# Performance work log

Hardware: AMD Instinct MI355X
Metric: run time of the kernel (lower is better)

Reference implementation:

```python
import jax, jax.numpy as jnp
import numpy as np

ALPHA = 0.7
NUM_HEADS = 12
NUM_KV_HEADS = 6
HEAD_DIM = 64
ROPE_BASE = 10000.0


def ternary_quantize(w):
    thr = ALPHA * jnp.mean(jnp.abs(w))
    return jnp.sign(w) * (jnp.abs(w) >= thr).astype(w.dtype)


def bitlinear(x, w):
    # forward: F.linear(x, ternary(w)) * mean(|w|)
    scale = jnp.mean(jnp.abs(w))
    qw = ternary_quantize(w)
    return (x @ qw.T) * scale


def rope_tables(seq_len, dim, dtype):
    inv_freq = 1.0 / (ROPE_BASE ** (jnp.arange(0, dim, 2, dtype=jnp.float32) / dim))
    t = jnp.arange(seq_len, dtype=jnp.float32)
    freqs = jnp.outer(t, inv_freq)            # [S, dim/2]
    emb = jnp.concatenate([freqs, freqs], -1)  # [S, dim]
    return jnp.cos(emb).astype(dtype), jnp.sin(emb).astype(dtype)


def rotate_half(x):
    x1, x2 = jnp.split(x, 2, axis=-1)
    return jnp.concatenate([-x2, x1], axis=-1)


def setup_inputs() -> dict:
    key = jax.random.key(0)
    ks = jax.random.split(key, 5)
    B, S, H = 2, 2048, 768
    return {
        "hidden_states": jax.random.normal(ks[0], (B, S, H), jnp.float32),
        "Wq": jax.random.normal(ks[1], (768, 768), jnp.float32) * 0.02,
        "Wk": jax.random.normal(ks[2], (384, 768), jnp.float32) * 0.02,
        "Wv": jax.random.normal(ks[3], (384, 768), jnp.float32) * 0.02,
        "Wo": jax.random.normal(ks[4], (768, 768), jnp.float32) * 0.02,
    }


def reference(hidden_states, Wq, Wk, Wv, Wo):
    B, S, H = hidden_states.shape
    nh, nkv, hd = NUM_HEADS, NUM_KV_HEADS, HEAD_DIM
    groups = nh // nkv

    q = bitlinear(hidden_states, Wq).reshape(B, S, nh, hd).transpose(0, 2, 1, 3)
    k = bitlinear(hidden_states, Wk).reshape(B, S, nkv, hd).transpose(0, 2, 1, 3)
    v = bitlinear(hidden_states, Wv).reshape(B, S, nkv, hd).transpose(0, 2, 1, 3)

    cos, sin = rope_tables(S, hd, hidden_states.dtype)  # [S, hd]
    cos = cos[None, None]  # [1,1,S,hd]
    sin = sin[None, None]
    q = q * cos + rotate_half(q) * sin
    k = k * cos + rotate_half(k) * sin

    # GQA: expand kv heads to full head count
    k = jnp.repeat(k, groups, axis=1)  # [B, nh, S, hd]
    v = jnp.repeat(v, groups, axis=1)

    scale = 1.0 / jnp.sqrt(jnp.asarray(hd, hidden_states.dtype))
    scores = jnp.einsum("bhsd,bhtd->bhst", q, k) * scale
    attn = jax.nn.softmax(scores, axis=-1)
    out = jnp.einsum("bhst,bhtd->bhsd", attn, v)
    out = out.transpose(0, 2, 1, 3).reshape(B, S, H)
    return bitlinear(out, Wo)
```

## Files before the change

### kernel.cpp

```cpp
#include <hip/hip_runtime.h>
#include <cmath>

typedef unsigned short u16;
typedef unsigned int u32;
typedef __bf16 bf16x2 __attribute__((ext_vector_type(2)));
typedef __bf16 bf16x8 __attribute__((ext_vector_type(8)));
typedef float f32x16 __attribute__((ext_vector_type(16)));

#define NQ (768*768)
#define NK (384*768)

__device__ __forceinline__ u16 f2bf(float f) {
  u32 u = __float_as_uint(f);
  u32 r = (u + 0x7FFFu + ((u >> 16) & 1u)) >> 16;
  return (u16)r;
}
__device__ __forceinline__ u32 packbf(float a, float b) {
#if __has_builtin(__builtin_amdgcn_cvt_pk_bf16_f32)
  bf16x2 v = __builtin_amdgcn_cvt_pk_bf16_f32(a, b);
  u32 r; __builtin_memcpy(&r, &v, 4); return r;
#else
  return (u32)f2bf(a) | ((u32)f2bf(b) << 16);
#endif
}
__device__ __forceinline__ float fexp2(float x) {
#if __has_builtin(__builtin_amdgcn_exp2f)
  return __builtin_amdgcn_exp2f(x);
#else
  return exp2f(x);
#endif
}
__device__ __forceinline__ bf16x8 ldfrag(const u16* p) { bf16x8 v; __builtin_memcpy(&v, p, 16); return v; }
__device__ __forceinline__ f32x16 mfma32_(bf16x8 a, bf16x8 b, f32x16 c) {
  return __builtin_amdgcn_mfma_f32_32x32x16_bf16(a, b, c, 0, 0, 0);
}

__device__ __forceinline__ int fidx(int r, int k) {
  return (r >> 5) * 24576 + (k >> 4) * 512 + ((r & 31) + 32 * ((k >> 3) & 1)) * 8 + (k & 7);
}
__device__ __forceinline__ int kidx(int b6kvh, int s, int d) {
  return b6kvh * 131072 + (s >> 5) * 2048 + (d >> 4) * 512 +
         ((s & 31) + 32 * ((d >> 3) & 1)) * 8 + (d & 7);
}
__device__ __forceinline__ int qidx(int b, int s, int h, int d) {
  return ((b * 64 + (s >> 5)) * 12 + h) * 2048 + (d >> 4) * 512 +
         ((s & 31) + 32 * ((d >> 3) & 1)) * 8 + (d & 7);
}
__device__ __forceinline__ int vidx(int b6kvh, int d, int p) {
  return b6kvh * 131072 + (p >> 6) * 4096 + (d >> 5) * 2048 + ((p >> 4) & 3) * 512 +
         ((d & 31) + 32 * ((p >> 3) & 1)) * 8 + (p & 7);
}

__global__ __launch_bounds__(256) void abssum_kernel(const float* __restrict__ wq, const float* __restrict__ wk,
                                                     const float* __restrict__ wv, const float* __restrict__ wo,
                                                     float* __restrict__ sums) {
  int which = blockIdx.y;
  const float* w = (which == 0) ? wq : (which == 1) ? wk : (which == 2) ? wv : wo;
  int n4 = ((which == 0 || which == 3) ? NQ : NK) >> 2;
  const float4* w4 = (const float4*)w;
  float s = 0.f;
  for (int i = blockIdx.x * blockDim.x + threadIdx.x; i < n4; i += gridDim.x * blockDim.x) {
    float4 v = w4[i];
    s += fabsf(v.x) + fabsf(v.y) + fabsf(v.z) + fabsf(v.w);
  }
  for (int off = 32; off; off >>= 1) s += __shfl_down(s, off);
  __shared__ float ls[4];
  if ((threadIdx.x & 63) == 0) ls[threadIdx.x >> 6] = s;
  __syncthreads();
  if (threadIdx.x == 0) atomicAdd(&sums[which], ls[0] + ls[1] + ls[2] + ls[3]);
}

__global__ __launch_bounds__(256) void prep_kernel(const float* __restrict__ wq, const float* __restrict__ wk,
                                                   const float* __restrict__ wv, const float* __restrict__ wo,
                                                   const float* __restrict__ sums, const float* __restrict__ x,
                                                   u16* __restrict__ qw, u16* __restrict__ woq,
                                                   u16* __restrict__ xb, float2* __restrict__ rt) {
  int i = blockIdx.x * blockDim.x + threadIdx.x;
  if (i < 221184) {
    int n = i / 96, k8 = i - n * 96;
    const float* src; float th; u16* dst; int nd;
    if (n < 768)       { src = wq + n * 768;          th = 0.7f * sums[0] * (1.f / NQ); dst = qw;  nd = n; }
    else if (n < 1152) { src = wk + (n - 768) * 768;  th = 0.7f * sums[1] * (1.f / NK); dst = qw;  nd = n; }
    else if (n < 1536) { src = wv + (n - 1152) * 768; th = 0.7f * sums[2] * (1.f / NK); dst = qw;  nd = n; }
    else               { src = wo + (n - 1536) * 768; th = 0.7f * sums[3] * (1.f / NQ); dst = woq; nd = n - 1536; }
    const float4* sp = (const float4*)(src + k8 * 8);
    float4 v0 = sp[0], v1 = sp[1];
    float e[8] = {v0.x, v0.y, v0.z, v0.w, v1.x, v1.y, v1.z, v1.w};
    u16 o[8];
#pragma unroll
    for (int j = 0; j < 8; j++)
      o[j] = f2bf((fabsf(e[j]) >= th) ? ((e[j] > 0.f) ? 1.f : -1.f) : 0.f);
    __builtin_memcpy(dst + fidx(nd, k8 * 8), o, 16);
  } else if (i < 614400) {
    int j = i - 221184;
    int m = j / 96, k8 = j - m * 96;
    const float4* xp = (const float4*)(x + m * 768 + k8 * 8);
    float4 v0 = xp[0], v1 = xp[1];
    u16 o[8] = { f2bf(v0.x), f2bf(v0.y), f2bf(v0.z), f2bf(v0.w),
                 f2bf(v1.x), f2bf(v1.y), f2bf(v1.z), f2bf(v1.w) };
    __builtin_memcpy(xb + fidx(m, k8 * 8), o, 16);
  } else {
    int j = i - 614400;
    int s = j >> 5, c = j & 31;
    float f = exp2f((float)c * -0.41524101186092029f);
    float sn, cs; sincosf((float)s * f, &sn, &cs);
    rt[j] = make_float2(cs, sn);
  }
}

__global__ __launch_bounds__(256, 3) void gemm_qkv_kernel(const u16* __restrict__ xb, const u16* __restrict__ qw,
                                                          const float* __restrict__ sums,
                                                          const float2* __restrict__ rt,
                                                          u16* __restrict__ qb, u16* __restrict__ kb,
                                                          u16* __restrict__ vT) {
  int tn = blockIdx.x, tm = blockIdx.y;
  int t = threadIdx.x, lane = t & 63, w = t >> 6, c = lane & 31, g2 = lane >> 5;
  int wm = w & 1, wn = w >> 1;
  const u16* abase = xb + (tm * 2 + wm) * 24576 + lane * 8;
  const u16* bbase0 = qw + (tn * 4 + wn * 2) * 24576 + lane * 8;
  const u16* bbase1 = bbase0 + 24576;
  f32x16 acc[2]; acc[0] = (f32x16)0.f; acc[1] = (f32x16)0.f;
  bf16x8 aA[4], c0A[4], c1A[4], aB[4], c0B[4], c1B[4];
#pragma unroll
  for (int ks = 0; ks < 4; ks++) {
    aA[ks]  = ldfrag(abase + ks * 512);
    c0A[ks] = ldfrag(bbase0 + ks * 512);
    c1A[ks] = ldfrag(bbase1 + ks * 512);
  }
#pragma unroll
  for (int kk = 0; kk < 48; kk += 8) {
#pragma unroll
    for (int ks = 0; ks < 4; ks++) {
      aB[ks]  = ldfrag(abase + (kk + 4 + ks) * 512);
      c0B[ks] = ldfrag(bbase0 + (kk + 4 + ks) * 512);
      c1B[ks] = ldfrag(bbase1 + (kk + 4 + ks) * 512);
    }
#pragma unroll
    for (int ks = 0; ks < 4; ks++) {
      acc[0] = mfma32_(aA[ks], c0A[ks], acc[0]);
      acc[1] = mfma32_(aA[ks], c1A[ks], acc[1]);
    }
    if (kk + 8 < 48) {
#pragma unroll
      for (int ks = 0; ks < 4; ks++) {
        aA[ks]  = ldfrag(abase + (kk + 8 + ks) * 512);
        c0A[ks] = ldfrag(bbase0 + (kk + 8 + ks) * 512);
        c1A[ks] = ldfrag(bbase1 + (kk + 8 + ks) * 512);
      }
    }
#pragma unroll
    for (int ks = 0; ks < 4; ks++) {
      acc[0] = mfma32_(aB[ks], c0B[ks], acc[0]);
      acc[1] = mfma32_(aB[ks], c1B[ks], acc[1]);
    }
  }
  float sq = sums[0] * (1.f / NQ) * 0.180336880111120f;
  float sk = sums[1] * (1.f / NK);
  float sv = sums[2] * (1.f / NK);
  int mb = tm * 64 + wm * 32 + 4 * g2;
  if (tn < 9) {
    float sc = (tn < 6) ? sq : sk;
    int head = (tn < 6) ? (tn * 2 + wn) : ((tn - 6) * 2 + wn);
    const float2* rp = rt + c;
#pragma unroll
    for (int r = 0; r < 16; r++) {
      int m = mb + (r & 3) + 8 * (r >> 2);
      int bb = m >> 11, s = m & 2047;
      float2 cs2 = rp[s << 5];
      float x1 = acc[0][r] * sc, x2 = acc[1][r] * sc;
      u16 y1 = f2bf(x1 * cs2.x - x2 * cs2.y);
      u16 y2 = f2bf(x2 * cs2.x + x1 * cs2.y);
      if (tn < 6) {
        qb[qidx(bb, s, head, c)]      = y1;
        qb[qidx(bb, s, head, c + 32)] = y2;
      } else {
        kb[kidx(bb * 6 + head, s, c)]      = y1;
        kb[kidx(bb * 6 + head, s, c + 32)] = y2;
      }
    }
  } else {
    int kvh = (tn - 9) * 2 + wn;
#pragma unroll
    for (int nb = 0; nb < 2; nb++)
#pragma unroll
      for (int r = 0; r < 16; r++) {
        int m = mb + (r & 3) + 8 * (r >> 2);
        int bb = m >> 11, s = m & 2047;
        int sp = (s & ~12) | ((s & 4) << 1) | ((s & 8) >> 1);
        vT[vidx(bb * 6 + kvh, nb * 32 + c, sp)] = f2bf(acc[nb][r] * sv);
      }
  }
}

__device__ __forceinline__ void attn_step(const bf16x8 (&kf)[4], const bf16x8 (&vf)[2][2],
                                          const bf16x8 (&qf)[4], f32x16 (&O)[2], float& lsum) {
  f32x16 S = (f32x16)0.f;
#pragma unroll
  for (int ks = 0; ks < 4; ks++) S = mfma32_(kf[ks], qf[ks], S);
#pragma unroll
  for (int r = 0; r < 16; r++) S[r] = fexp2(S[r]);
  lsum += (((S[0] + S[1]) + (S[2] + S[3])) + ((S[4] + S[5]) + (S[6] + S[7])))
        + (((S[8] + S[9]) + (S[10] + S[11])) + ((S[12] + S[13]) + (S[14] + S[15])));
  u32 P[8];
#pragma unroll
  for (int j = 0; j < 8; j++) P[j] = packbf(S[2 * j], S[2 * j + 1]);
  bf16x8 PA0, PA1;
  __builtin_memcpy(&PA0, &P[0], 16);
  __builtin_memcpy(&PA1, &P[4], 16);
  O[0] = mfma32_(PA0, vf[0][0], O[0]);
  O[1] = mfma32_(PA0, vf[1][0], O[1]);
  O[0] = mfma32_(PA1, vf[0][1], O[0]);
  O[1] = mfma32_(PA1, vf[1][1], O[1]);
}

__global__ __launch_bounds__(256, 3) void attn_kernel(const u16* __restrict__ qb, const u16* __restrict__ kb,
                                                      const u16* __restrict__ vT, u16* __restrict__ ab) {
  __shared__ float Obuf[4][32][66];
  __shared__ float Lbuf[4][32];
  int bk = blockIdx.x;
  int b = bk / 6, kvh = bk % 6;
  int qp = blockIdx.y & 31, h2 = blockIdx.y >> 5;
  int h = kvh * 2 + h2;
  int t = threadIdx.x, lane = t & 63, w = t >> 6, c = lane & 31, g2 = lane >> 5;

  const u16* q0 = qb + ((b * 64 + qp * 2) * 12 + h) * 2048 + lane * 8;
  const u16* q1 = q0 + 12 * 2048;
  bf16x8 qf0[4], qf1[4];
#pragma unroll
  for (int ks = 0; ks < 4; ks++) { qf0[ks] = ldfrag(q0 + ks * 512); qf1[ks] = ldfrag(q1 + ks * 512); }

  f32x16 fz = (f32x16)0.f;
  f32x16 O0[2] = {fz, fz}, O1[2] = {fz, fz};
  float lsum0 = 0.f, lsum1 = 0.f;

  const u16* Kb = kb + bk * 131072;
  const u16* Vb = vT + bk * 131072;

  for (int it = 0; it < 16; ++it) {
    int g = w * 16 + it;
    const u16* kt = Kb + g * 2048 + lane * 8;
    const u16* vt = Vb + (g >> 1) * 4096 + (g & 1) * 1024 + lane * 8;
    bf16x8 kf[4], vf[2][2];
#pragma unroll
    for (int ks = 0; ks < 4; ks++) kf[ks] = ldfrag(kt + ks * 512);
#pragma unroll
    for (int dn = 0; dn < 2; dn++)
#pragma unroll
      for (int ksv = 0; ksv < 2; ksv++)
        vf[dn][ksv] = ldfrag(vt + dn * 2048 + ksv * 512);
    attn_step(kf, vf, qf0, O0, lsum0);
    attn_step(kf, vf, qf1, O1, lsum1);
  }

  float lt0 = lsum0 + __shfl_xor(lsum0, 32);
  float lt1 = lsum1 + __shfl_xor(lsum1, 32);

#pragma unroll
  for (int qi = 0; qi < 2; qi++) {
    if (qi) __syncthreads();
    if (g2 == 0) Lbuf[w][c] = qi ? lt1 : lt0;
    const f32x16* Ow = qi ? O1 : O0;
#pragma unroll
    for (int dn = 0; dn < 2; dn++)
#pragma unroll
      for (int r = 0; r < 16; r++)
        Obuf[w][(r & 3) + 8 * (r >> 2) + 4 * g2][dn * 32 + c] = Ow[dn][r];
    __syncthreads();
    int qq = t >> 3, col8 = (t & 7) * 8;
    float l = Lbuf[0][qq] + Lbuf[1][qq] + Lbuf[2][qq] + Lbuf[3][qq];
    float inv = 1.f / l;
    u16 o[8];
#pragma unroll
    for (int j = 0; j < 8; j++)
      o[j] = f2bf((Obuf[0][qq][col8 + j] + Obuf[1][qq][col8 + j] +
                   Obuf[2][qq][col8 + j] + Obuf[3][qq][col8 + j]) * inv);
    int mg = b * 64 + qp * 2 + qi;
    u16* dst = ab + mg * 24576 + ((h * 64 + col8) >> 4) * 512 + ((col8 >> 3) & 1) * 256 + qq * 8;
    __builtin_memcpy(dst, o, 16);
  }
}

__global__ __launch_bounds__(256, 3) void gemm_out_kernel(const u16* __restrict__ ab, const u16* __restrict__ woq,
                                                          const float* __restrict__ sums, float* __restrict__ out) {
  int tn = blockIdx.x, tm = blockIdx.y;
  int t = threadIdx.x, lane = t & 63, w = t >> 6, c = lane & 31, g2 = lane >> 5;
  int wm = w & 1, wn = w >> 1;
  const u16* abase = ab + (tm * 2 + wm) * 24576 + lane * 8;
  const u16* bbase = woq + (tn * 2 + wn) * 24576 + lane * 8;
  f32x16 acc = (f32x16)0.f;
  bf16x8 aA[4], bA[4], aB[4], bB[4];
#pragma unroll
  for (int ks = 0; ks < 4; ks++) {
    aA[ks] = ldfrag(abase + ks * 512);
    bA[ks] = ldfrag(bbase + ks * 512);
  }
#pragma unroll
  for (int kk = 0; kk < 48; kk += 8) {
#pragma unroll
    for (int ks = 0; ks < 4; ks++) {
      aB[ks] = ldfrag(abase + (kk + 4 + ks) * 512);
      bB[ks] = ldfrag(bbase + (kk + 4 + ks) * 512);
    }
#pragma unroll
    for (int ks = 0; ks < 4; ks++) acc = mfma32_(aA[ks], bA[ks], acc);
    if (kk + 8 < 48) {
#pragma unroll
      for (int ks = 0; ks < 4; ks++) {
        aA[ks] = ldfrag(abase + (kk + 8 + ks) * 512);
        bA[ks] = ldfrag(bbase + (kk + 8 + ks) * 512);
      }
    }
#pragma unroll
    for (int ks = 0; ks < 4; ks++) acc = mfma32_(aB[ks], bB[ks], acc);
  }
  float so = sums[3] * (1.f / NQ);
  int mb = tm * 64 + wm * 32 + 4 * g2;
#pragma unroll
  for (int r = 0; r < 16; r++) {
    int m = mb + (r & 3) + 8 * (r >> 2);
    out[m * 768 + tn * 64 + wn * 32 + c] = acc[r] * so;
  }
}

extern "C" void kernel_launch(void* const* d_in, const int* in_sizes, int n_in,
                              void* d_out, int out_size, void* d_ws, size_t ws_size,
                              hipStream_t stream) {
  const float* x  = (const float*)d_in[0];
  const float* wq = (const float*)d_in[1];
  const float* wk = (const float*)d_in[2];
  const float* wv = (const float*)d_in[3];
  const float* wo = (const float*)d_in[4];
  float* out = (float*)d_out;
  char* ws = (char*)d_ws;

  float* sums = (float*)ws;
  u16* qw  = (u16*)(ws + 256);
  u16* woq = (u16*)(ws + 2359552);
  u16* xb  = (u16*)(ws + 3539200);
  u16* qb  = (u16*)(ws + 9830656);
  u16* kb  = (u16*)(ws + 16122112);
  u16* vT  = (u16*)(ws + 19267840);
  u16* ab  = (u16*)(ws + 22413568);
  float2* rt = (float2*)(ws + 28705024);

  hipMemsetAsync(sums, 0, 16, stream);
  dim3 blk(256);
  abssum_kernel<<<dim3(64, 4), blk, 0, stream>>>(wq, wk, wv, wo, sums);
  prep_kernel<<<dim3(2656), blk, 0, stream>>>(wq, wk, wv, wo, sums, x, qw, woq, xb, rt);
  gemm_qkv_kernel<<<dim3(12, 64), blk, 0, stream>>>(xb, qw, sums, rt, qb, kb, vT);
  attn_kernel<<<dim3(12, 64), blk, 0, stream>>>(qb, kb, vT, ab);
  gemm_out_kernel<<<dim3(12, 64), blk, 0, stream>>>(ab, woq, sums, out);
}
```

Measured before the change: 154.8 us.

## Stage QKV GEMM tiles through LDS with async loads and add MFMA priority hints

The QKV projection GEMM now loads A and B tiles into double-buffered shared memory with global_load_lds, and each block computes a 128x128 tile with a 2x2 accumulator grid per wave. This halves the grid in M and cuts redundant global fragment loads. The attention step also raises wave priority around its MFMA groups with s_setprio and sums the row totals with packed two-wide float adds. The trade-off is more LDS use, a barrier every k-step, and lower occupancy (launch bound 2 instead of 3).

```diff
diff --git a/kernel.cpp b/kernel.cpp
--- a/kernel.cpp
+++ b/kernel.cpp
@@ -5,6 +5,7 @@
 typedef unsigned int u32;
 typedef __bf16 bf16x2 __attribute__((ext_vector_type(2)));
 typedef __bf16 bf16x8 __attribute__((ext_vector_type(8)));
+typedef float f32x2 __attribute__((ext_vector_type(2)));
 typedef float f32x16 __attribute__((ext_vector_type(16)));
 
 #define NQ (768*768)
@@ -33,6 +34,10 @@
 __device__ __forceinline__ bf16x8 ldfrag(const u16* p) { bf16x8 v; __builtin_memcpy(&v, p, 16); return v; }
 __device__ __forceinline__ f32x16 mfma32_(bf16x8 a, bf16x8 b, f32x16 c) {
   return __builtin_amdgcn_mfma_f32_32x32x16_bf16(a, b, c, 0, 0, 0);
+}
+__device__ __forceinline__ void gload_lds16(const u16* g, u16* l) {
+  __builtin_amdgcn_global_load_lds((const __attribute__((address_space(1))) void*)g,
+                                   (__attribute__((address_space(3))) void*)l, 16, 0, 0);
 }
 
 __device__ __forceinline__ int fidx(int r, int k) {
@@ -108,109 +113,127 @@
   }
 }
 
-__global__ __launch_bounds__(256, 3) void gemm_qkv_kernel(const u16* __restrict__ xb, const u16* __restrict__ qw,
+__global__ __launch_bounds__(256, 2) void gemm_qkv_kernel(const u16* __restrict__ xb, const u16* __restrict__ qw,
                                                           const float* __restrict__ sums,
                                                           const float2* __restrict__ rt,
                                                           u16* __restrict__ qb, u16* __restrict__ kb,
                                                           u16* __restrict__ vT) {
+  __shared__ u16 sA[2][4][4][512];
+  __shared__ u16 sB[2][4][4][512];
   int tn = blockIdx.x, tm = blockIdx.y;
   int t = threadIdx.x, lane = t & 63, w = t >> 6, c = lane & 31, g2 = lane >> 5;
   int wm = w & 1, wn = w >> 1;
-  const u16* abase = xb + (tm * 2 + wm) * 24576 + lane * 8;
-  const u16* bbase0 = qw + (tn * 4 + wn * 2) * 24576 + lane * 8;
-  const u16* bbase1 = bbase0 + 24576;
-  f32x16 acc[2]; acc[0] = (f32x16)0.f; acc[1] = (f32x16)0.f;
-  bf16x8 aA[4], c0A[4], c1A[4], aB[4], c0B[4], c1B[4];
-#pragma unroll
-  for (int ks = 0; ks < 4; ks++) {
-    aA[ks]  = ldfrag(abase + ks * 512);
-    c0A[ks] = ldfrag(bbase0 + ks * 512);
-    c1A[ks] = ldfrag(bbase1 + ks * 512);
-  }
-#pragma unroll
-  for (int kk = 0; kk < 48; kk += 8) {
-#pragma unroll
-    for (int ks = 0; ks < 4; ks++) {
-      aB[ks]  = ldfrag(abase + (kk + 4 + ks) * 512);
-      c0B[ks] = ldfrag(bbase0 + (kk + 4 + ks) * 512);
-      c1B[ks] = ldfrag(bbase1 + (kk + 4 + ks) * 512);
-    }
-#pragma unroll
-    for (int ks = 0; ks < 4; ks++) {
-      acc[0] = mfma32_(aA[ks], c0A[ks], acc[0]);
-      acc[1] = mfma32_(aA[ks], c1A[ks], acc[1]);
-    }
-    if (kk + 8 < 48) {
-#pragma unroll
-      for (int ks = 0; ks < 4; ks++) {
-        aA[ks]  = ldfrag(abase + (kk + 8 + ks) * 512);
-        c0A[ks] = ldfrag(bbase0 + (kk + 8 + ks) * 512);
-        c1A[ks] = ldfrag(bbase1 + (kk + 8 + ks) * 512);
-      }
-    }
-#pragma unroll
-    for (int ks = 0; ks < 4; ks++) {
-      acc[0] = mfma32_(aB[ks], c0B[ks], acc[0]);
-      acc[1] = mfma32_(aB[ks], c1B[ks], acc[1]);
-    }
-  }
+
+  const u16* asrc = xb + (tm * 4 + w) * 24576 + lane * 8;
+  const u16* bsrc = qw + (tn * 4 + w) * 24576 + lane * 8;
+
+  auto stage = [&](int s, int bufi) {
+    u16* adst = &sA[bufi][w][0][0];
+    u16* bdst = &sB[bufi][w][0][0];
+    const u16* ap = asrc + s * 2048;
+    const u16* bp = bsrc + s * 2048;
+#pragma unroll
+    for (int kc = 0; kc < 4; kc++) {
+      gload_lds16(ap + kc * 512, adst + kc * 512);
+      gload_lds16(bp + kc * 512, bdst + kc * 512);
+    }
+  };
+
+  f32x16 acc[2][2];
+  acc[0][0] = (f32x16)0.f; acc[0][1] = (f32x16)0.f;
+  acc[1][0] = (f32x16)0.f; acc[1][1] = (f32x16)0.f;
+
+  stage(0, 0);
+  __syncthreads();
+  for (int s = 0; s < 12; ++s) {
+    int b = s & 1;
+    if (s < 11) stage(s + 1, b ^ 1);
+#pragma unroll
+    for (int kc = 0; kc < 4; kc++) {
+      bf16x8 a0 = ldfrag(&sA[b][2 * wm][kc][lane * 8]);
+      bf16x8 a1 = ldfrag(&sA[b][2 * wm + 1][kc][lane * 8]);
+      bf16x8 b0 = ldfrag(&sB[b][2 * wn][kc][lane * 8]);
+      bf16x8 b1 = ldfrag(&sB[b][2 * wn + 1][kc][lane * 8]);
+      acc[0][0] = mfma32_(a0, b0, acc[0][0]);
+      acc[0][1] = mfma32_(a0, b1, acc[0][1]);
+      acc[1][0] = mfma32_(a1, b0, acc[1][0]);
+      acc[1][1] = mfma32_(a1, b1, acc[1][1]);
+    }
+    __syncthreads();
+  }
+
   float sq = sums[0] * (1.f / NQ) * 0.180336880111120f;
   float sk = sums[1] * (1.f / NK);
   float sv = sums[2] * (1.f / NK);
-  int mb = tm * 64 + wm * 32 + 4 * g2;
   if (tn < 9) {
     float sc = (tn < 6) ? sq : sk;
     int head = (tn < 6) ? (tn * 2 + wn) : ((tn - 6) * 2 + wn);
     const float2* rp = rt + c;
 #pragma unroll
-    for (int r = 0; r < 16; r++) {
-      int m = mb + (r & 3) + 8 * (r >> 2);
-      int bb = m >> 11, s = m & 2047;
-      float2 cs2 = rp[s << 5];
-      float x1 = acc[0][r] * sc, x2 = acc[1][r] * sc;
-      u16 y1 = f2bf(x1 * cs2.x - x2 * cs2.y);
-      u16 y2 = f2bf(x2 * cs2.x + x1 * cs2.y);
-      if (tn < 6) {
-        qb[qidx(bb, s, head, c)]      = y1;
-        qb[qidx(bb, s, head, c + 32)] = y2;
-      } else {
-        kb[kidx(bb * 6 + head, s, c)]      = y1;
-        kb[kidx(bb * 6 + head, s, c + 32)] = y2;
-      }
-    }
-  } else {
-    int kvh = (tn - 9) * 2 + wn;
-#pragma unroll
-    for (int nb = 0; nb < 2; nb++)
+    for (int mi = 0; mi < 2; mi++) {
+      int mb = tm * 128 + wm * 64 + mi * 32 + 4 * g2;
 #pragma unroll
       for (int r = 0; r < 16; r++) {
         int m = mb + (r & 3) + 8 * (r >> 2);
         int bb = m >> 11, s = m & 2047;
-        int sp = (s & ~12) | ((s & 4) << 1) | ((s & 8) >> 1);
-        vT[vidx(bb * 6 + kvh, nb * 32 + c, sp)] = f2bf(acc[nb][r] * sv);
+        float2 cs2 = rp[s << 5];
+        float x1 = acc[mi][0][r] * sc, x2 = acc[mi][1][r] * sc;
+        u16 y1 = f2bf(x1 * cs2.x - x2 * cs2.y);
+        u16 y2 = f2bf(x2 * cs2.x + x1 * cs2.y);
+        if (tn < 6) {
+          qb[qidx(bb, s, head, c)]      = y1;
+          qb[qidx(bb, s, head, c + 32)] = y2;
+        } else {
+          kb[kidx(bb * 6 + head, s, c)]      = y1;
+          kb[kidx(bb * 6 + head, s, c + 32)] = y2;
+        }
       }
+    }
+  } else {
+    int kvh = (tn - 9) * 2 + wn;
+#pragma unroll
+    for (int mi = 0; mi < 2; mi++) {
+      int mb = tm * 128 + wm * 64 + mi * 32 + 4 * g2;
+#pragma unroll
+      for (int nb = 0; nb < 2; nb++)
+#pragma unroll
+        for (int r = 0; r < 16; r++) {
+          int m = mb + (r & 3) + 8 * (r >> 2);
+          int bb = m >> 11, s = m & 2047;
+          int sp = (s & ~12) | ((s & 4) << 1) | ((s & 8) >> 1);
+          vT[vidx(bb * 6 + kvh, nb * 32 + c, sp)] = f2bf(acc[mi][nb][r] * sv);
+        }
+    }
   }
 }
 
 __device__ __forceinline__ void attn_step(const bf16x8 (&kf)[4], const bf16x8 (&vf)[2][2],
                                           const bf16x8 (&qf)[4], f32x16 (&O)[2], float& lsum) {
   f32x16 S = (f32x16)0.f;
+  __builtin_amdgcn_s_setprio(1);
 #pragma unroll
   for (int ks = 0; ks < 4; ks++) S = mfma32_(kf[ks], qf[ks], S);
+  __builtin_amdgcn_s_setprio(0);
 #pragma unroll
   for (int r = 0; r < 16; r++) S[r] = fexp2(S[r]);
-  lsum += (((S[0] + S[1]) + (S[2] + S[3])) + ((S[4] + S[5]) + (S[6] + S[7])))
-        + (((S[8] + S[9]) + (S[10] + S[11])) + ((S[12] + S[13]) + (S[14] + S[15])));
+  f32x2 a0 = {S[0], S[1]},  a1 = {S[2], S[3]},  a2 = {S[4], S[5]},  a3 = {S[6], S[7]};
+  f32x2 a4 = {S[8], S[9]},  a5 = {S[10], S[11]}, a6 = {S[12], S[13]}, a7 = {S[14], S[15]};
+  f32x2 b0 = a0 + a1, b1 = a2 + a3, b2 = a4 + a5, b3 = a6 + a7;
+  f32x2 c0 = b0 + b1, c1 = b2 + b3;
+  f32x2 d = c0 + c1;
+  lsum += d.x + d.y;
   u32 P[8];
 #pragma unroll
   for (int j = 0; j < 8; j++) P[j] = packbf(S[2 * j], S[2 * j + 1]);
   bf16x8 PA0, PA1;
   __builtin_memcpy(&PA0, &P[0], 16);
   __builtin_memcpy(&PA1, &P[4], 16);
+  __builtin_amdgcn_s_setprio(1);
   O[0] = mfma32_(PA0, vf[0][0], O[0]);
   O[1] = mfma32_(PA0, vf[1][0], O[1]);
   O[0] = mfma32_(PA1, vf[0][1], O[0]);
   O[1] = mfma32_(PA1, vf[1][1], O[1]);
+  __builtin_amdgcn_s_setprio(0);
 }
 
 __global__ __launch_bounds__(256, 3) void attn_kernel(const u16* __restrict__ qb, const u16* __restrict__ kb,
@@ -347,7 +370,7 @@
   dim3 blk(256);
   abssum_kernel<<<dim3(64, 4), blk, 0, stream>>>(wq, wk, wv, wo, sums);
   prep_kernel<<<dim3(2656), blk, 0, stream>>>(wq, wk, wv, wo, sums, x, qw, woq, xb, rt);
-  gemm_qkv_kernel<<<dim3(12, 64), blk, 0, stream>>>(xb, qw, sums, rt, qb, kb, vT);
+  gemm_qkv_kernel<<<dim3(12, 32), blk, 0, stream>>>(xb, qw, sums, rt, qb, kb, vT);
   attn_kernel<<<dim3(12, 64), blk, 0, stream>>>(qb, kb, vT, ab);
   gemm_out_kernel<<<dim3(12, 64), blk, 0, stream>>>(ab, woq, sums, out);
 }
```

Result: no change. 153.4 us (-1.0%).
